# Kernel tuning notes

Hardware: AMD Instinct MI355X
Metric: run time of the kernel (lower is better)

## Reference

```python
import jax, jax.numpy as jnp
import numpy as np

B, S, D, E = 4, 2048, 512, 32

def setup_inputs() -> dict:
    key = jax.random.key(0)
    k1, k2, k3 = jax.random.split(key, 3)
    x = jax.random.normal(k1, (B, S, D), dtype=jnp.float32)
    # glorot-ish scaling for weights
    gate_w = jax.random.normal(k2, (D, E), dtype=jnp.float32) * (1.0 / np.sqrt(D))
    gate_b = jnp.zeros((E,), dtype=jnp.float32)
    expert_w = jax.random.normal(k3, (E, D, D), dtype=jnp.float32) * (1.0 / np.sqrt(D))
    return {"x": x, "gate_w": gate_w, "gate_b": gate_b, "expert_w": expert_w}

def reference(x, gate_w, gate_b, expert_w):
    # gate_scores: [B,S,E] (context=None -> route on x itself)
    gate = jax.nn.softmax(jnp.einsum('bsd,de->bse', x, gate_w) + gate_b, axis=-1)
    # Dense soft-MoE: sum_e gate[b,s,e] * (x[b,s,:] @ expert_w[e])
    # Single einsum avoids materializing the [B,S,E,D] intermediate.
    out = jnp.einsum('bse,bsd,edf->bsf', gate, x, expert_w)
    return out
```

## Files before the change

kernel.cpp:

```cpp
#include <hip/hip_runtime.h>

#define TOK 8192
#define DIM 512
#define NE  32
#define KTOT (NE * DIM)

#define BM 256
#define BN 128
#define BK 64

typedef float f32x4  __attribute__((ext_vector_type(4)));
typedef float f32x16 __attribute__((ext_vector_type(16)));
typedef short s16x8  __attribute__((ext_vector_type(8)));

typedef const void __attribute__((address_space(1)))* gp1_t;
typedef void __attribute__((address_space(3)))* lp3_t;

__device__ __forceinline__ void gl_lds16(const void* g, void* l) {
    __builtin_amdgcn_global_load_lds((gp1_t)g, (lp3_t)l, 16, 0, 0);
}

__device__ __forceinline__ void stageA(const ushort* g, char* l) {
    gl_lds16(g,                      l);
    gl_lds16(g + (size_t) 64 * DIM,  l + 8192);
    gl_lds16(g + (size_t)128 * DIM,  l + 16384);
    gl_lds16(g + (size_t)192 * DIM,  l + 24576);
}
__device__ __forceinline__ void stageB(const ushort* g, char* l) {
    gl_lds16(g,                      l);
    gl_lds16(g + (size_t)64 * KTOT,  l + 8192);
}

__device__ __forceinline__ ushort f2bf(float f) {
    unsigned u = __builtin_bit_cast(unsigned, f);
    unsigned r = (u + 0x7fffu + ((u >> 16) & 1u)) >> 16;
    return (ushort)r;
}

__global__ __launch_bounds__(256) void k_prep(const float* __restrict__ w,
                                              ushort* __restrict__ wt,
                                              const float* __restrict__ x,
                                              const float* __restrict__ gw,
                                              const float* __restrict__ gb,
                                              float* __restrict__ G,
                                              ushort* __restrict__ xb) {
    __shared__ __align__(16) char smem[64 * 65 * 4];
    const int bx = blockIdx.x;
    const int tid = threadIdx.x;
    if (bx < 2048) {
        float (*tile)[65] = (float(*)[65])smem;
        const int e = bx >> 6;
        const int f0 = ((bx >> 3) & 7) * 64;
        const int d0 = (bx & 7) * 64;
        const int tx = tid & 63, ty = tid >> 6;
        const float* we = w + (size_t)e * DIM * DIM;
#pragma unroll
        for (int i = ty; i < 64; i += 4)
            tile[i][tx] = we[(size_t)(d0 + i) * DIM + f0 + tx];
        __syncthreads();
#pragma unroll
        for (int i = ty; i < 64; i += 4)
            wt[(size_t)(f0 + i) * KTOT + e * DIM + d0 + tx] = f2bf(tile[tx][i]);
    } else {
        float* xs = (float*)smem;
        const int t0 = (bx - 2048) * 8;
        const float* xBase = x + (size_t)t0 * DIM;
#pragma unroll
        for (int k = 0; k < 4; ++k) {
            int i4 = (k * 256 + tid) * 4;
            float4 v = *(const float4*)(xBase + i4);
            xs[i4 + 0] = v.x; xs[i4 + 1] = v.y; xs[i4 + 2] = v.z; xs[i4 + 3] = v.w;
            ushort4 o;
            o.x = f2bf(v.x); o.y = f2bf(v.y); o.z = f2bf(v.z); o.w = f2bf(v.w);
            *(ushort4*)(xb + (size_t)t0 * DIM + i4) = o;
        }
        __syncthreads();
        const int tok = tid >> 5;
        const int e = tid & 31;
        float l = gb[e];
        const float* xr = xs + tok * DIM;
#pragma unroll 8
        for (int d = 0; d < DIM; ++d)
            l += xr[d] * gw[d * NE + e];
        float mx = l;
#pragma unroll
        for (int m = 16; m >= 1; m >>= 1) mx = fmaxf(mx, __shfl_xor(mx, m));
        float ex = expf(l - mx);
        float s = ex;
#pragma unroll
        for (int m = 16; m >= 1; m >>= 1) s += __shfl_xor(s, m);
        G[(size_t)(t0 + tok) * NE + e] = ex / s;
    }
}

__global__ __launch_bounds__(512, 2) void k_moe_gemm(const ushort* __restrict__ xb,
                                                     const ushort* __restrict__ wt,
                                                     const float* __restrict__ G,
                                                     float* __restrict__ out0,
                                                     float* __restrict__ out1) {
    __shared__ __align__(16) ushort As[2][BM * BK];
    __shared__ __align__(16) ushort Bs[2][BN * BK];
    __shared__ float Gs[16][BM];

    const int tid = threadIdx.x;
    const int m0 = blockIdx.y * BM;
    const int n0 = blockIdx.x * BN;
    const int e0 = blockIdx.z * 16;
    float* __restrict__ dst = blockIdx.z ? out1 : out0;

    for (int i = tid; i < 16 * BM; i += 512) {
        int e = i >> 8, r = i & 255;
        Gs[e][r] = G[(size_t)(m0 + r) * NE + e0 + e];
    }

    const int lane = tid & 63;
    const int wave = tid >> 6;
    const int wm = (wave & 3) * 64;
    const int wn = (wave >> 2) * 64;
    const int l31 = lane & 31;
    const int hi = lane >> 5;
    const int key = l31 & 7;

    int chunkOff[4], rowOffA[2], rowOffB[2];
#pragma unroll
    for (int s = 0; s < 4; ++s) chunkOff[s] = ((2 * s + hi) ^ key) * 16;
#pragma unroll
    for (int i = 0; i < 2; ++i) {
        rowOffA[i] = (wm + i * 32 + l31) * 128;
        rowOffB[i] = (wn + i * 32 + l31) * 128;
    }

    const int srow = tid >> 3;
    const int scol = ((tid & 7) ^ (srow & 7)) * 8;
    const ushort* aBase = xb + (size_t)(m0 + srow) * DIM + scol;
    const ushort* bBase = wt + (size_t)(n0 + srow) * KTOT + (size_t)e0 * DIM + scol;
    const int ldsOff = tid * 16;

    f32x16 zv16;
#pragma unroll
    for (int j = 0; j < 16; ++j) zv16[j] = 0.f;
    f32x16 acc[2][2];
#pragma unroll
    for (int i = 0; i < 2; ++i)
#pragma unroll
        for (int j = 0; j < 2; ++j) acc[i][j] = zv16;

    stageA(aBase, (char*)As[0] + ldsOff);
    stageB(bBase, (char*)Bs[0] + ldsOff);
    __syncthreads();

#pragma unroll 1
    for (int kt = 0; kt < 8; ++kt) {
        const char* Ab = (const char*)As[kt & 1];
        s16x8 areg[2][4];
#pragma unroll
        for (int mi = 0; mi < 2; ++mi)
#pragma unroll
            for (int s = 0; s < 4; ++s)
                areg[mi][s] = *(const s16x8*)(Ab + rowOffA[mi] + chunkOff[s]);

#pragma unroll 1
        for (int ee = 0; ee < 16; ++ee) {
            const int gn = kt * 16 + ee + 1;
            if (gn < 128) {
                const ushort* bN = bBase + (size_t)(gn & 15) * DIM + (gn >> 4) * BK;
                stageB(bN, (char*)Bs[gn & 1] + ldsOff);
                if (ee == 15)
                    stageA(aBase + (kt + 1) * BK, (char*)As[(kt + 1) & 1] + ldsOff);
            }

            const char* Bb = (const char*)Bs[ee & 1];
            s16x8 breg[2][4];
#pragma unroll
            for (int nj = 0; nj < 2; ++nj)
#pragma unroll
                for (int s = 0; s < 4; ++s)
                    breg[nj][s] = *(const s16x8*)(Bb + rowOffB[nj] + chunkOff[s]);

#pragma unroll
            for (int mi = 0; mi < 2; ++mi) {
                f32x16 p0 = __builtin_amdgcn_mfma_f32_32x32x16_bf16(areg[mi][0], breg[0][0], zv16, 0, 0, 0);
                f32x16 p1 = __builtin_amdgcn_mfma_f32_32x32x16_bf16(areg[mi][0], breg[1][0], zv16, 0, 0, 0);
#pragma unroll
                for (int s = 1; s < 4; ++s) {
                    p0 = __builtin_amdgcn_mfma_f32_32x32x16_bf16(areg[mi][s], breg[0][s], p0, 0, 0, 0);
                    p1 = __builtin_amdgcn_mfma_f32_32x32x16_bf16(areg[mi][s], breg[1][s], p1, 0, 0, 0);
                }
#pragma unroll
                for (int gq = 0; gq < 4; ++gq) {
                    const f32x4 gt = *(const f32x4*)&Gs[ee][wm + mi * 32 + 8 * gq + 4 * hi];
#pragma unroll
                    for (int j = 0; j < 4; ++j) {
                        acc[mi][0][4 * gq + j] += gt[j] * p0[4 * gq + j];
                        acc[mi][1][4 * gq + j] += gt[j] * p1[4 * gq + j];
                    }
                }
            }
            __syncthreads();
        }
    }

#pragma unroll
    for (int mi = 0; mi < 2; ++mi)
#pragma unroll
        for (int nj = 0; nj < 2; ++nj) {
            const int col = n0 + wn + nj * 32 + l31;
#pragma unroll
            for (int gq = 0; gq < 4; ++gq) {
                float* p = dst + (size_t)(m0 + wm + mi * 32 + 8 * gq + 4 * hi) * DIM + col;
                p[0 * DIM] = acc[mi][nj][4 * gq + 0];
                p[1 * DIM] = acc[mi][nj][4 * gq + 1];
                p[2 * DIM] = acc[mi][nj][4 * gq + 2];
                p[3 * DIM] = acc[mi][nj][4 * gq + 3];
            }
        }
}

__global__ __launch_bounds__(256) void k_reduce(float* __restrict__ out,
                                                const float* __restrict__ P) {
    int i = (blockIdx.x * 256 + threadIdx.x) * 4;
    float4 a = *(const float4*)(out + i);
    float4 b = *(const float4*)(P + i);
    a.x += b.x; a.y += b.y; a.z += b.z; a.w += b.w;
    *(float4*)(out + i) = a;
}

extern "C" void kernel_launch(void* const* d_in, const int* in_sizes, int n_in,
                              void* d_out, int out_size, void* d_ws, size_t ws_size,
                              hipStream_t stream) {
    const float* x  = (const float*)d_in[0];
    const float* gw = (const float*)d_in[1];
    const float* gb = (const float*)d_in[2];
    const float* w  = (const float*)d_in[3];
    float* out = (float*)d_out;

    char* ws = (char*)d_ws;
    ushort* xb = (ushort*)ws;
    ushort* wt = (ushort*)(ws + (8u << 20));
    float*  G  = (float*)(ws + (24u << 20));
    float*  P  = (float*)(ws + (25u << 20));

    k_prep<<<dim3(2048 + TOK / 8), dim3(256), 0, stream>>>(w, wt, x, gw, gb, G, xb);
    k_moe_gemm<<<dim3(DIM / BN, TOK / BM, 2), dim3(512), 0, stream>>>(xb, wt, G, out, P);
    k_reduce<<<dim3(TOK * DIM / 1024), dim3(256), 0, stream>>>(out, P);
}
```

Before: 262.1 us.

## Double K tile to 128 and single-buffer A with register-held fragments

Raises BK from 64 to 128, halving the number of K-tile/expert iterations. Each per-expert inner step now issues 8 MFMAs per accumulator chain before the gate-weighted accumulation, so that fixed cost is paid half as often. A is single-buffered and loaded into registers at ee==0, with the next A tile prefetched at ee==1. The MFMA loop is reordered by n, and the gate values are hoisted into registers once per step. The larger LDS footprint and register pressure (areg of 16 vectors, breg of 8) may reduce occupancy at the 512,2 launch bound. The A overwrite timing also depends on barriers placed correctly between the register loads and the restaging.

```diff
diff --git a/kernel.cpp b/kernel.cpp
--- a/kernel.cpp
+++ b/kernel.cpp
@@ -7,7 +7,7 @@
 
 #define BM 256
 #define BN 128
-#define BK 64
+#define BK 128
 
 typedef float f32x4  __attribute__((ext_vector_type(4)));
 typedef float f32x16 __attribute__((ext_vector_type(16)));
@@ -21,14 +21,14 @@
 }
 
 __device__ __forceinline__ void stageA(const ushort* g, char* l) {
-    gl_lds16(g,                      l);
-    gl_lds16(g + (size_t) 64 * DIM,  l + 8192);
-    gl_lds16(g + (size_t)128 * DIM,  l + 16384);
-    gl_lds16(g + (size_t)192 * DIM,  l + 24576);
+#pragma unroll
+    for (int r = 0; r < 8; ++r)
+        gl_lds16(g + (size_t)r * 32 * DIM, l + r * 8192);
 }
 __device__ __forceinline__ void stageB(const ushort* g, char* l) {
-    gl_lds16(g,                      l);
-    gl_lds16(g + (size_t)64 * KTOT,  l + 8192);
+#pragma unroll
+    for (int r = 0; r < 4; ++r)
+        gl_lds16(g + (size_t)r * 32 * KTOT, l + r * 8192);
 }
 
 __device__ __forceinline__ ushort f2bf(float f) {
@@ -98,7 +98,7 @@
                                                      const float* __restrict__ G,
                                                      float* __restrict__ out0,
                                                      float* __restrict__ out1) {
-    __shared__ __align__(16) ushort As[2][BM * BK];
+    __shared__ __align__(16) ushort As[BM * BK];
     __shared__ __align__(16) ushort Bs[2][BN * BK];
     __shared__ float Gs[16][BM];
 
@@ -121,17 +121,17 @@
     const int hi = lane >> 5;
     const int key = l31 & 7;
 
-    int chunkOff[4], rowOffA[2], rowOffB[2];
-#pragma unroll
-    for (int s = 0; s < 4; ++s) chunkOff[s] = ((2 * s + hi) ^ key) * 16;
+    int chunkOff[8], rowOffA[2], rowOffB[2];
+#pragma unroll
+    for (int s = 0; s < 8; ++s) chunkOff[s] = ((2 * s + hi) ^ key) * 16;
 #pragma unroll
     for (int i = 0; i < 2; ++i) {
-        rowOffA[i] = (wm + i * 32 + l31) * 128;
-        rowOffB[i] = (wn + i * 32 + l31) * 128;
-    }
-
-    const int srow = tid >> 3;
-    const int scol = ((tid & 7) ^ (srow & 7)) * 8;
+        rowOffA[i] = (wm + i * 32 + l31) * 256;
+        rowOffB[i] = (wn + i * 32 + l31) * 256;
+    }
+
+    const int srow = tid >> 4;
+    const int scol = ((tid & 15) ^ (srow & 7)) * 8;
     const ushort* aBase = xb + (size_t)(m0 + srow) * DIM + scol;
     const ushort* bBase = wt + (size_t)(n0 + srow) * KTOT + (size_t)e0 * DIM + scol;
     const int ldsOff = tid * 16;
@@ -145,54 +145,62 @@
 #pragma unroll
         for (int j = 0; j < 2; ++j) acc[i][j] = zv16;
 
-    stageA(aBase, (char*)As[0] + ldsOff);
+    stageA(aBase, (char*)As + ldsOff);
     stageB(bBase, (char*)Bs[0] + ldsOff);
     __syncthreads();
 
+    s16x8 areg[2][8];
+
 #pragma unroll 1
-    for (int kt = 0; kt < 8; ++kt) {
-        const char* Ab = (const char*)As[kt & 1];
-        s16x8 areg[2][4];
-#pragma unroll
-        for (int mi = 0; mi < 2; ++mi)
-#pragma unroll
-            for (int s = 0; s < 4; ++s)
-                areg[mi][s] = *(const s16x8*)(Ab + rowOffA[mi] + chunkOff[s]);
-
+    for (int kt = 0; kt < 4; ++kt) {
 #pragma unroll 1
         for (int ee = 0; ee < 16; ++ee) {
-            const int gn = kt * 16 + ee + 1;
-            if (gn < 128) {
+            const int g = kt * 16 + ee;
+
+            const int gn = g + 1;
+            if (gn < 64) {
                 const ushort* bN = bBase + (size_t)(gn & 15) * DIM + (gn >> 4) * BK;
                 stageB(bN, (char*)Bs[gn & 1] + ldsOff);
-                if (ee == 15)
-                    stageA(aBase + (kt + 1) * BK, (char*)As[(kt + 1) & 1] + ldsOff);
-            }
-
-            const char* Bb = (const char*)Bs[ee & 1];
-            s16x8 breg[2][4];
-#pragma unroll
-            for (int nj = 0; nj < 2; ++nj)
-#pragma unroll
-                for (int s = 0; s < 4; ++s)
-                    breg[nj][s] = *(const s16x8*)(Bb + rowOffB[nj] + chunkOff[s]);
-
-#pragma unroll
-            for (int mi = 0; mi < 2; ++mi) {
-                f32x16 p0 = __builtin_amdgcn_mfma_f32_32x32x16_bf16(areg[mi][0], breg[0][0], zv16, 0, 0, 0);
-                f32x16 p1 = __builtin_amdgcn_mfma_f32_32x32x16_bf16(areg[mi][0], breg[1][0], zv16, 0, 0, 0);
-#pragma unroll
-                for (int s = 1; s < 4; ++s) {
-                    p0 = __builtin_amdgcn_mfma_f32_32x32x16_bf16(areg[mi][s], breg[0][s], p0, 0, 0, 0);
-                    p1 = __builtin_amdgcn_mfma_f32_32x32x16_bf16(areg[mi][s], breg[1][s], p1, 0, 0, 0);
+            }
+            if (ee == 1 && kt < 3)
+                stageA(aBase + (kt + 1) * BK, (char*)As + ldsOff);
+
+            if (ee == 0) {
+#pragma unroll
+                for (int mi = 0; mi < 2; ++mi)
+#pragma unroll
+                    for (int s = 0; s < 8; ++s)
+                        areg[mi][s] = *(const s16x8*)((const char*)As + rowOffA[mi] + chunkOff[s]);
+            }
+
+            f32x4 greg[2][4];
+#pragma unroll
+            for (int mi = 0; mi < 2; ++mi)
+#pragma unroll
+                for (int gq = 0; gq < 4; ++gq)
+                    greg[mi][gq] = *(const f32x4*)&Gs[ee][wm + mi * 32 + 8 * gq + 4 * hi];
+
+            const char* Bb = (const char*)Bs[g & 1];
+#pragma unroll
+            for (int nj = 0; nj < 2; ++nj) {
+                s16x8 breg[8];
+#pragma unroll
+                for (int s = 0; s < 8; ++s)
+                    breg[s] = *(const s16x8*)(Bb + rowOffB[nj] + chunkOff[s]);
+
+                f32x16 p0 = __builtin_amdgcn_mfma_f32_32x32x16_bf16(areg[0][0], breg[0], zv16, 0, 0, 0);
+                f32x16 p1 = __builtin_amdgcn_mfma_f32_32x32x16_bf16(areg[1][0], breg[0], zv16, 0, 0, 0);
+#pragma unroll
+                for (int s = 1; s < 8; ++s) {
+                    p0 = __builtin_amdgcn_mfma_f32_32x32x16_bf16(areg[0][s], breg[s], p0, 0, 0, 0);
+                    p1 = __builtin_amdgcn_mfma_f32_32x32x16_bf16(areg[1][s], breg[s], p1, 0, 0, 0);
                 }
 #pragma unroll
                 for (int gq = 0; gq < 4; ++gq) {
-                    const f32x4 gt = *(const f32x4*)&Gs[ee][wm + mi * 32 + 8 * gq + 4 * hi];
 #pragma unroll
                     for (int j = 0; j < 4; ++j) {
-                        acc[mi][0][4 * gq + j] += gt[j] * p0[4 * gq + j];
-                        acc[mi][1][4 * gq + j] += gt[j] * p1[4 * gq + j];
+                        acc[0][nj][4 * gq + j] += greg[0][gq][j] * p0[4 * gq + j];
+                        acc[1][nj][4 * gq + j] += greg[1][gq][j] * p1[4 * gq + j];
                     }
                 }
             }
```

Result: faster. 256.8 us (-2.1%).

## Drop expert split-K and reduce kernel; use 64-row tiles over all experts

Applied to the files above, without the earlier changes.

Each GEMM block now covers all 32 experts for a 64x128 output tile with 4 waves, in place of splitting experts across two z-slices into a partial buffer. This removes the separate reduce kernel and the partial-output write and read. The grid becomes 4x128 blocks of 256 threads, and the gate values are loaded into registers before the MFMAs. The cost is less A-tile reuse per block: each wave computes 64x32, so B traffic from global memory per unit of output rises.

```diff
diff --git a/kernel.cpp b/kernel.cpp
--- a/kernel.cpp
+++ b/kernel.cpp
@@ -5,7 +5,7 @@
 #define NE  32
 #define KTOT (NE * DIM)
 
-#define BM 256
+#define BM 64
 #define BN 128
 #define BK 64
 
@@ -21,14 +21,13 @@
 }
 
 __device__ __forceinline__ void stageA(const ushort* g, char* l) {
-    gl_lds16(g,                      l);
-    gl_lds16(g + (size_t) 64 * DIM,  l + 8192);
-    gl_lds16(g + (size_t)128 * DIM,  l + 16384);
-    gl_lds16(g + (size_t)192 * DIM,  l + 24576);
+    gl_lds16(g,                     l);
+    gl_lds16(g + (size_t)32 * DIM,  l + 4096);
 }
 __device__ __forceinline__ void stageB(const ushort* g, char* l) {
-    gl_lds16(g,                      l);
-    gl_lds16(g + (size_t)64 * KTOT,  l + 8192);
+#pragma unroll
+    for (int r = 0; r < 4; ++r)
+        gl_lds16(g + (size_t)r * 32 * KTOT, l + r * 4096);
 }
 
 __device__ __forceinline__ ushort f2bf(float f) {
@@ -93,57 +92,48 @@
     }
 }
 
-__global__ __launch_bounds__(512, 2) void k_moe_gemm(const ushort* __restrict__ xb,
+__global__ __launch_bounds__(256, 2) void k_moe_gemm(const ushort* __restrict__ xb,
                                                      const ushort* __restrict__ wt,
                                                      const float* __restrict__ G,
-                                                     float* __restrict__ out0,
-                                                     float* __restrict__ out1) {
+                                                     float* __restrict__ out) {
     __shared__ __align__(16) ushort As[2][BM * BK];
     __shared__ __align__(16) ushort Bs[2][BN * BK];
-    __shared__ float Gs[16][BM];
+    __shared__ float Gs[NE][BM];
 
     const int tid = threadIdx.x;
     const int m0 = blockIdx.y * BM;
     const int n0 = blockIdx.x * BN;
-    const int e0 = blockIdx.z * 16;
-    float* __restrict__ dst = blockIdx.z ? out1 : out0;
-
-    for (int i = tid; i < 16 * BM; i += 512) {
-        int e = i >> 8, r = i & 255;
-        Gs[e][r] = G[(size_t)(m0 + r) * NE + e0 + e];
+
+    for (int i = tid; i < NE * BM; i += 256) {
+        int e = i >> 6, r = i & 63;
+        Gs[e][r] = G[(size_t)(m0 + r) * NE + e];
     }
 
     const int lane = tid & 63;
     const int wave = tid >> 6;
-    const int wm = (wave & 3) * 64;
-    const int wn = (wave >> 2) * 64;
+    const int wn = wave * 32;
     const int l31 = lane & 31;
     const int hi = lane >> 5;
     const int key = l31 & 7;
 
-    int chunkOff[4], rowOffA[2], rowOffB[2];
+    int chunkOff[4];
 #pragma unroll
     for (int s = 0; s < 4; ++s) chunkOff[s] = ((2 * s + hi) ^ key) * 16;
-#pragma unroll
-    for (int i = 0; i < 2; ++i) {
-        rowOffA[i] = (wm + i * 32 + l31) * 128;
-        rowOffB[i] = (wn + i * 32 + l31) * 128;
-    }
+    const int rowOffA0 = (l31) * 128;
+    const int rowOffA1 = (32 + l31) * 128;
+    const int rowOffB  = (wn + l31) * 128;
 
     const int srow = tid >> 3;
     const int scol = ((tid & 7) ^ (srow & 7)) * 8;
     const ushort* aBase = xb + (size_t)(m0 + srow) * DIM + scol;
-    const ushort* bBase = wt + (size_t)(n0 + srow) * KTOT + (size_t)e0 * DIM + scol;
+    const ushort* bBase = wt + (size_t)(n0 + srow) * KTOT + scol;
     const int ldsOff = tid * 16;
 
     f32x16 zv16;
 #pragma unroll
     for (int j = 0; j < 16; ++j) zv16[j] = 0.f;
-    f32x16 acc[2][2];
-#pragma unroll
-    for (int i = 0; i < 2; ++i)
-#pragma unroll
-        for (int j = 0; j < 2; ++j) acc[i][j] = zv16;
+    f32x16 acc[2];
+    acc[0] = zv16; acc[1] = zv16;
 
     stageA(aBase, (char*)As[0] + ldsOff);
     stageB(bBase, (char*)Bs[0] + ldsOff);
@@ -154,46 +144,47 @@
         const char* Ab = (const char*)As[kt & 1];
         s16x8 areg[2][4];
 #pragma unroll
-        for (int mi = 0; mi < 2; ++mi)
-#pragma unroll
-            for (int s = 0; s < 4; ++s)
-                areg[mi][s] = *(const s16x8*)(Ab + rowOffA[mi] + chunkOff[s]);
+        for (int s = 0; s < 4; ++s) {
+            areg[0][s] = *(const s16x8*)(Ab + rowOffA0 + chunkOff[s]);
+            areg[1][s] = *(const s16x8*)(Ab + rowOffA1 + chunkOff[s]);
+        }
 
 #pragma unroll 1
-        for (int ee = 0; ee < 16; ++ee) {
-            const int gn = kt * 16 + ee + 1;
-            if (gn < 128) {
-                const ushort* bN = bBase + (size_t)(gn & 15) * DIM + (gn >> 4) * BK;
+        for (int ee = 0; ee < NE; ++ee) {
+            const int gn = kt * NE + ee + 1;
+            if (gn < 8 * NE) {
+                const ushort* bN = bBase + (size_t)(gn & 31) * DIM + (gn >> 5) * BK;
                 stageB(bN, (char*)Bs[gn & 1] + ldsOff);
-                if (ee == 15)
+                if (ee == NE - 1)
                     stageA(aBase + (kt + 1) * BK, (char*)As[(kt + 1) & 1] + ldsOff);
             }
 
             const char* Bb = (const char*)Bs[ee & 1];
-            s16x8 breg[2][4];
-#pragma unroll
-            for (int nj = 0; nj < 2; ++nj)
-#pragma unroll
-                for (int s = 0; s < 4; ++s)
-                    breg[nj][s] = *(const s16x8*)(Bb + rowOffB[nj] + chunkOff[s]);
-
-#pragma unroll
-            for (int mi = 0; mi < 2; ++mi) {
-                f32x16 p0 = __builtin_amdgcn_mfma_f32_32x32x16_bf16(areg[mi][0], breg[0][0], zv16, 0, 0, 0);
-                f32x16 p1 = __builtin_amdgcn_mfma_f32_32x32x16_bf16(areg[mi][0], breg[1][0], zv16, 0, 0, 0);
-#pragma unroll
-                for (int s = 1; s < 4; ++s) {
-                    p0 = __builtin_amdgcn_mfma_f32_32x32x16_bf16(areg[mi][s], breg[0][s], p0, 0, 0, 0);
-                    p1 = __builtin_amdgcn_mfma_f32_32x32x16_bf16(areg[mi][s], breg[1][s], p1, 0, 0, 0);
-                }
-#pragma unroll
-                for (int gq = 0; gq < 4; ++gq) {
-                    const f32x4 gt = *(const f32x4*)&Gs[ee][wm + mi * 32 + 8 * gq + 4 * hi];
-#pragma unroll
-                    for (int j = 0; j < 4; ++j) {
-                        acc[mi][0][4 * gq + j] += gt[j] * p0[4 * gq + j];
-                        acc[mi][1][4 * gq + j] += gt[j] * p1[4 * gq + j];
-                    }
+            s16x8 breg[4];
+#pragma unroll
+            for (int s = 0; s < 4; ++s)
+                breg[s] = *(const s16x8*)(Bb + rowOffB + chunkOff[s]);
+
+            f32x4 greg[2][4];
+#pragma unroll
+            for (int mi = 0; mi < 2; ++mi)
+#pragma unroll
+                for (int gq = 0; gq < 4; ++gq)
+                    greg[mi][gq] = *(const f32x4*)&Gs[ee][mi * 32 + 8 * gq + 4 * hi];
+
+            f32x16 p0 = __builtin_amdgcn_mfma_f32_32x32x16_bf16(areg[0][0], breg[0], zv16, 0, 0, 0);
+            f32x16 p1 = __builtin_amdgcn_mfma_f32_32x32x16_bf16(areg[1][0], breg[0], zv16, 0, 0, 0);
+#pragma unroll
+            for (int s = 1; s < 4; ++s) {
+                p0 = __builtin_amdgcn_mfma_f32_32x32x16_bf16(areg[0][s], breg[s], p0, 0, 0, 0);
+                p1 = __builtin_amdgcn_mfma_f32_32x32x16_bf16(areg[1][s], breg[s], p1, 0, 0, 0);
+            }
+#pragma unroll
+            for (int gq = 0; gq < 4; ++gq) {
+#pragma unroll
+                for (int j = 0; j < 4; ++j) {
+                    acc[0][4 * gq + j] += greg[0][gq][j] * p0[4 * gq + j];
+                    acc[1][4 * gq + j] += greg[1][gq][j] * p1[4 * gq + j];
                 }
             }
             __syncthreads();
@@ -201,28 +192,17 @@
     }
 
 #pragma unroll
-    for (int mi = 0; mi < 2; ++mi)
-#pragma unroll
-        for (int nj = 0; nj < 2; ++nj) {
-            const int col = n0 + wn + nj * 32 + l31;
-#pragma unroll
-            for (int gq = 0; gq < 4; ++gq) {
-                float* p = dst + (size_t)(m0 + wm + mi * 32 + 8 * gq + 4 * hi) * DIM + col;
-                p[0 * DIM] = acc[mi][nj][4 * gq + 0];
-                p[1 * DIM] = acc[mi][nj][4 * gq + 1];
-                p[2 * DIM] = acc[mi][nj][4 * gq + 2];
-                p[3 * DIM] = acc[mi][nj][4 * gq + 3];
-            }
-        }
-}
-
-__global__ __launch_bounds__(256) void k_reduce(float* __restrict__ out,
-                                                const float* __restrict__ P) {
-    int i = (blockIdx.x * 256 + threadIdx.x) * 4;
-    float4 a = *(const float4*)(out + i);
-    float4 b = *(const float4*)(P + i);
-    a.x += b.x; a.y += b.y; a.z += b.z; a.w += b.w;
-    *(float4*)(out + i) = a;
+    for (int mi = 0; mi < 2; ++mi) {
+        const int col = n0 + wn + l31;
+#pragma unroll
+        for (int gq = 0; gq < 4; ++gq) {
+            float* p = out + (size_t)(m0 + mi * 32 + 8 * gq + 4 * hi) * DIM + col;
+            p[0 * DIM] = acc[mi][4 * gq + 0];
+            p[1 * DIM] = acc[mi][4 * gq + 1];
+            p[2 * DIM] = acc[mi][4 * gq + 2];
+            p[3 * DIM] = acc[mi][4 * gq + 3];
+        }
+    }
 }
 
 extern "C" void kernel_launch(void* const* d_in, const int* in_sizes, int n_in,
@@ -238,9 +218,7 @@
     ushort* xb = (ushort*)ws;
     ushort* wt = (ushort*)(ws + (8u << 20));
     float*  G  = (float*)(ws + (24u << 20));
-    float*  P  = (float*)(ws + (25u << 20));
 
     k_prep<<<dim3(2048 + TOK / 8), dim3(256), 0, stream>>>(w, wt, x, gw, gb, G, xb);
-    k_moe_gemm<<<dim3(DIM / BN, TOK / BM, 2), dim3(512), 0, stream>>>(xb, wt, G, out, P);
-    k_reduce<<<dim3(TOK * DIM / 1024), dim3(256), 0, stream>>>(out, P);
-}
+    k_moe_gemm<<<dim3(DIM / BN, TOK / BM), dim3(256), 0, stream>>>(xb, wt, G, out);
+}
```

Result: slower. 272.9 us (+4.1%).

## Restructure MoE GEMM into 128x128 tiles with ping-pong LDS pipeline and barriers

Applied to the files above, without the earlier changes.

Halves the M tile to 128, remaps waves to 2x4 with 64x32 per-wave tiles, and rewrites the main loop as 64 iterations over (expert, 128-wide K chunk). Each iteration is split into four phases with explicit s_barrier, waitcnt, sched_barrier and setprio so that global-to-LDS loads overlap MFMA work. The aim is to hide memory latency and raise occupancy or grid parallelism. The cost is more barriers, more A reloads because of the smaller M tile, and fragile hand-tuned wait counts.

```diff
diff --git a/kernel.cpp b/kernel.cpp
--- a/kernel.cpp
+++ b/kernel.cpp
@@ -5,7 +5,7 @@
 #define NE  32
 #define KTOT (NE * DIM)
 
-#define BM 256
+#define BM 128
 #define BN 128
 #define BK 64
 
@@ -20,15 +20,9 @@
     __builtin_amdgcn_global_load_lds((gp1_t)g, (lp3_t)l, 16, 0, 0);
 }
 
-__device__ __forceinline__ void stageA(const ushort* g, char* l) {
-    gl_lds16(g,                      l);
-    gl_lds16(g + (size_t) 64 * DIM,  l + 8192);
-    gl_lds16(g + (size_t)128 * DIM,  l + 16384);
-    gl_lds16(g + (size_t)192 * DIM,  l + 24576);
-}
-__device__ __forceinline__ void stageB(const ushort* g, char* l) {
-    gl_lds16(g,                      l);
-    gl_lds16(g + (size_t)64 * KTOT,  l + 8192);
+__device__ __forceinline__ void stage2(const ushort* g, size_t rstride, char* l) {
+    gl_lds16(g,                 l);
+    gl_lds16(g + 64 * rstride,  l + 8192);
 }
 
 __device__ __forceinline__ ushort f2bf(float f) {
@@ -98,8 +92,8 @@
                                                      const float* __restrict__ G,
                                                      float* __restrict__ out0,
                                                      float* __restrict__ out1) {
-    __shared__ __align__(16) ushort As[2][BM * BK];
-    __shared__ __align__(16) ushort Bs[2][BN * BK];
+    __shared__ __align__(16) ushort As[2][2][BM * BK];
+    __shared__ __align__(16) ushort Bs[2][2][BN * BK];
     __shared__ float Gs[16][BM];
 
     const int tid = threadIdx.x;
@@ -108,27 +102,25 @@
     const int e0 = blockIdx.z * 16;
     float* __restrict__ dst = blockIdx.z ? out1 : out0;
 
-    for (int i = tid; i < 16 * BM; i += 512) {
-        int e = i >> 8, r = i & 255;
+    for (int idx = tid; idx < 16 * BM; idx += 512) {
+        int e = idx >> 7, r = idx & 127;
         Gs[e][r] = G[(size_t)(m0 + r) * NE + e0 + e];
     }
 
     const int lane = tid & 63;
     const int wave = tid >> 6;
-    const int wm = (wave & 3) * 64;
-    const int wn = (wave >> 2) * 64;
+    const int wm = (wave >> 2) * 64;
+    const int wn = (wave & 3) * 32;
     const int l31 = lane & 31;
     const int hi = lane >> 5;
     const int key = l31 & 7;
 
-    int chunkOff[4], rowOffA[2], rowOffB[2];
+    int chunkOff[4];
 #pragma unroll
     for (int s = 0; s < 4; ++s) chunkOff[s] = ((2 * s + hi) ^ key) * 16;
-#pragma unroll
-    for (int i = 0; i < 2; ++i) {
-        rowOffA[i] = (wm + i * 32 + l31) * 128;
-        rowOffB[i] = (wn + i * 32 + l31) * 128;
-    }
+    const int rowA0 = (wm + l31) * 128;
+    const int rowA1 = (wm + 32 + l31) * 128;
+    const int rowB  = (wn + l31) * 128;
 
     const int srow = tid >> 3;
     const int scol = ((tid & 7) ^ (srow & 7)) * 8;
@@ -139,81 +131,124 @@
     f32x16 zv16;
 #pragma unroll
     for (int j = 0; j < 16; ++j) zv16[j] = 0.f;
-    f32x16 acc[2][2];
-#pragma unroll
-    for (int i = 0; i < 2; ++i)
-#pragma unroll
-        for (int j = 0; j < 2; ++j) acc[i][j] = zv16;
-
-    stageA(aBase, (char*)As[0] + ldsOff);
-    stageB(bBase, (char*)Bs[0] + ldsOff);
-    __syncthreads();
+    f32x16 accA = zv16, accB = zv16;
+    f32x16 paccA, paccB;
+
+    stage2(aBase,      DIM,  (char*)As[0][0] + ldsOff);
+    stage2(bBase,      KTOT, (char*)Bs[0][0] + ldsOff);
+    stage2(aBase + 64, DIM,  (char*)As[0][1] + ldsOff);
+    stage2(bBase + 64, KTOT, (char*)Bs[0][1] + ldsOff);
+    asm volatile("s_waitcnt vmcnt(4) lgkmcnt(0)" ::: "memory");
+    __builtin_amdgcn_s_barrier();
+
+    s16x8 areg[4], breg[4];
 
 #pragma unroll 1
-    for (int kt = 0; kt < 8; ++kt) {
-        const char* Ab = (const char*)As[kt & 1];
-        s16x8 areg[2][4];
-#pragma unroll
-        for (int mi = 0; mi < 2; ++mi)
-#pragma unroll
-            for (int s = 0; s < 4; ++s)
-                areg[mi][s] = *(const s16x8*)(Ab + rowOffA[mi] + chunkOff[s]);
-
-#pragma unroll 1
-        for (int ee = 0; ee < 16; ++ee) {
-            const int gn = kt * 16 + ee + 1;
-            if (gn < 128) {
-                const ushort* bN = bBase + (size_t)(gn & 15) * DIM + (gn >> 4) * BK;
-                stageB(bN, (char*)Bs[gn & 1] + ldsOff);
-                if (ee == 15)
-                    stageA(aBase + (kt + 1) * BK, (char*)As[(kt + 1) & 1] + ldsOff);
-            }
-
-            const char* Bb = (const char*)Bs[ee & 1];
-            s16x8 breg[2][4];
-#pragma unroll
-            for (int nj = 0; nj < 2; ++nj)
-#pragma unroll
-                for (int s = 0; s < 4; ++s)
-                    breg[nj][s] = *(const s16x8*)(Bb + rowOffB[nj] + chunkOff[s]);
-
-#pragma unroll
-            for (int mi = 0; mi < 2; ++mi) {
-                f32x16 p0 = __builtin_amdgcn_mfma_f32_32x32x16_bf16(areg[mi][0], breg[0][0], zv16, 0, 0, 0);
-                f32x16 p1 = __builtin_amdgcn_mfma_f32_32x32x16_bf16(areg[mi][0], breg[1][0], zv16, 0, 0, 0);
-#pragma unroll
-                for (int s = 1; s < 4; ++s) {
-                    p0 = __builtin_amdgcn_mfma_f32_32x32x16_bf16(areg[mi][s], breg[0][s], p0, 0, 0, 0);
-                    p1 = __builtin_amdgcn_mfma_f32_32x32x16_bf16(areg[mi][s], breg[1][s], p1, 0, 0, 0);
-                }
-#pragma unroll
-                for (int gq = 0; gq < 4; ++gq) {
-                    const f32x4 gt = *(const f32x4*)&Gs[ee][wm + mi * 32 + 8 * gq + 4 * hi];
-#pragma unroll
-                    for (int j = 0; j < 4; ++j) {
-                        acc[mi][0][4 * gq + j] += gt[j] * p0[4 * gq + j];
-                        acc[mi][1][4 * gq + j] += gt[j] * p1[4 * gq + j];
-                    }
+    for (int i = 0; i < 64; ++i) {
+        const int d  = i & 1;
+        const int p  = i & 3;
+        const int el = i >> 2;
+        const int i1 = i + 1;
+        const bool st = (i1 < 64);
+        const int dn = i1 & 1;
+        const ushort* aN = aBase + (i1 & 3) * 128;
+        const ushort* bN = bBase + (size_t)(i1 >> 2) * DIM + (i1 & 3) * 128;
+        const char* At0 = (const char*)As[d][0];
+        const char* At1 = (const char*)As[d][1];
+        const char* Bt0 = (const char*)Bs[d][0];
+        const char* Bt1 = (const char*)Bs[d][1];
+
+#pragma unroll
+        for (int s = 0; s < 4; ++s) {
+            areg[s] = *(const s16x8*)(At0 + rowA0 + chunkOff[s]);
+            breg[s] = *(const s16x8*)(Bt0 + rowB + chunkOff[s]);
+        }
+        if (st) stage2(aN, DIM, (char*)As[dn][0] + ldsOff);
+        __builtin_amdgcn_s_barrier();
+        asm volatile("s_waitcnt lgkmcnt(0)" ::: "memory");
+        __builtin_amdgcn_sched_barrier(0);
+        __builtin_amdgcn_s_setprio(1);
+        paccA = __builtin_amdgcn_mfma_f32_32x32x16_bf16(areg[0], breg[0],
+                    (p == 0) ? zv16 : paccA, 0, 0, 0);
+#pragma unroll
+        for (int s = 1; s < 4; ++s)
+            paccA = __builtin_amdgcn_mfma_f32_32x32x16_bf16(areg[s], breg[s], paccA, 0, 0, 0);
+        __builtin_amdgcn_s_setprio(0);
+        __builtin_amdgcn_s_barrier();
+
+#pragma unroll
+        for (int s = 0; s < 4; ++s)
+            areg[s] = *(const s16x8*)(At0 + rowA1 + chunkOff[s]);
+        if (st) stage2(bN, KTOT, (char*)Bs[dn][0] + ldsOff);
+        __builtin_amdgcn_s_barrier();
+        asm volatile("s_waitcnt lgkmcnt(0)" ::: "memory");
+        __builtin_amdgcn_sched_barrier(0);
+        __builtin_amdgcn_s_setprio(1);
+        paccB = __builtin_amdgcn_mfma_f32_32x32x16_bf16(areg[0], breg[0],
+                    (p == 0) ? zv16 : paccB, 0, 0, 0);
+#pragma unroll
+        for (int s = 1; s < 4; ++s)
+            paccB = __builtin_amdgcn_mfma_f32_32x32x16_bf16(areg[s], breg[s], paccB, 0, 0, 0);
+        __builtin_amdgcn_s_setprio(0);
+        if (i == 63) asm volatile("s_waitcnt vmcnt(0)" ::: "memory");
+        else         asm volatile("s_waitcnt vmcnt(4)" ::: "memory");
+        __builtin_amdgcn_s_barrier();
+
+#pragma unroll
+        for (int s = 0; s < 4; ++s) {
+            areg[s] = *(const s16x8*)(At1 + rowA0 + chunkOff[s]);
+            breg[s] = *(const s16x8*)(Bt1 + rowB + chunkOff[s]);
+        }
+        if (st) stage2(aN + 64, DIM, (char*)As[dn][1] + ldsOff);
+        __builtin_amdgcn_s_barrier();
+        asm volatile("s_waitcnt lgkmcnt(0)" ::: "memory");
+        __builtin_amdgcn_sched_barrier(0);
+        __builtin_amdgcn_s_setprio(1);
+#pragma unroll
+        for (int s = 0; s < 4; ++s)
+            paccA = __builtin_amdgcn_mfma_f32_32x32x16_bf16(areg[s], breg[s], paccA, 0, 0, 0);
+        __builtin_amdgcn_s_setprio(0);
+        __builtin_amdgcn_s_barrier();
+
+#pragma unroll
+        for (int s = 0; s < 4; ++s)
+            areg[s] = *(const s16x8*)(At1 + rowA1 + chunkOff[s]);
+        if (st) stage2(bN + 64, KTOT, (char*)Bs[dn][1] + ldsOff);
+        __builtin_amdgcn_s_barrier();
+        asm volatile("s_waitcnt lgkmcnt(0)" ::: "memory");
+        __builtin_amdgcn_sched_barrier(0);
+        __builtin_amdgcn_s_setprio(1);
+#pragma unroll
+        for (int s = 0; s < 4; ++s)
+            paccB = __builtin_amdgcn_mfma_f32_32x32x16_bf16(areg[s], breg[s], paccB, 0, 0, 0);
+        __builtin_amdgcn_s_setprio(0);
+        if (p == 3) {
+#pragma unroll
+            for (int gq = 0; gq < 4; ++gq) {
+                const f32x4 gA = *(const f32x4*)&Gs[el][wm + 8 * gq + 4 * hi];
+                const f32x4 gB = *(const f32x4*)&Gs[el][wm + 32 + 8 * gq + 4 * hi];
+#pragma unroll
+                for (int j = 0; j < 4; ++j) {
+                    accA[4 * gq + j] += gA[j] * paccA[4 * gq + j];
+                    accB[4 * gq + j] += gB[j] * paccB[4 * gq + j];
                 }
             }
-            __syncthreads();
-        }
-    }
-
-#pragma unroll
-    for (int mi = 0; mi < 2; ++mi)
-#pragma unroll
-        for (int nj = 0; nj < 2; ++nj) {
-            const int col = n0 + wn + nj * 32 + l31;
-#pragma unroll
-            for (int gq = 0; gq < 4; ++gq) {
-                float* p = dst + (size_t)(m0 + wm + mi * 32 + 8 * gq + 4 * hi) * DIM + col;
-                p[0 * DIM] = acc[mi][nj][4 * gq + 0];
-                p[1 * DIM] = acc[mi][nj][4 * gq + 1];
-                p[2 * DIM] = acc[mi][nj][4 * gq + 2];
-                p[3 * DIM] = acc[mi][nj][4 * gq + 3];
-            }
-        }
+        }
+        asm volatile("s_waitcnt vmcnt(4)" ::: "memory");
+        __builtin_amdgcn_s_barrier();
+    }
+
+    const int col = n0 + wn + l31;
+#pragma unroll
+    for (int gq = 0; gq < 4; ++gq) {
+        float* pA = dst + (size_t)(m0 + wm + 8 * gq + 4 * hi) * DIM + col;
+        float* pB = dst + (size_t)(m0 + wm + 32 + 8 * gq + 4 * hi) * DIM + col;
+#pragma unroll
+        for (int j = 0; j < 4; ++j) {
+            pA[j * DIM] = accA[4 * gq + j];
+            pB[j * DIM] = accB[4 * gq + j];
+        }
+    }
 }
 
 __global__ __launch_bounds__(256) void k_reduce(float* __restrict__ out,
```

New measurement: 318.7 us. 21.6% more time.
